# Performance work log

Measured on AMD Instinct MI355X. Metric: run time of the kernel, lower is better.

## Reference

```python
import jax, jax.numpy as jnp
import numpy as np

B, T, SEG = 64, 16, 50          # batch, n segments, segment length (cap 50 in original)
E, D, H, F = 512, 512, 8, 2048  # dim_embeddings, dim_encoder, n_heads, dim_ff
DH = D // H
SCALE = float(1.0 / np.sqrt(DH))


def _ln(x, g, b):
    m = jnp.mean(x, -1, keepdims=True)
    v = jnp.var(x, -1, keepdims=True)
    return (x - m) * jax.lax.rsqrt(v + 1e-5) * g + b


def _mha(q_in, kv_in, Wq, Wk, Wv, Wo, kv_lens):
    b, sq, _ = q_in.shape
    sk = kv_in.shape[1]
    q = (q_in @ Wq).reshape(b, sq, H, DH)
    k = (kv_in @ Wk).reshape(b, sk, H, DH)
    v = (kv_in @ Wv).reshape(b, sk, H, DH)
    scores = jnp.einsum('bqhd,bkhd->bhqk', q, k) * SCALE
    mask = jnp.arange(sk)[None, :] < kv_lens[:, None]  # [b, sk] key-padding mask
    scores = jnp.where(mask[:, None, None, :], scores, -1e9)
    a = jax.nn.softmax(scores, axis=-1)
    o = jnp.einsum('bhqk,bkhd->bqhd', a, v).reshape(b, sq, D)
    return o @ Wo


def _ffn(x, W1, W2):
    return jax.nn.relu(x @ W1) @ W2


def _encoder(x, lens, p):
    # TransformerEncoder: project E->D, masked self-attn + FFN, post-LN residuals
    h = x @ p['eWin']
    h = _ln(h + _mha(h, h, p['eWq'], p['eWk'], p['eWv'], p['eWo'], lens), p['eG1'], p['eB1'])
    return _ln(h + _ffn(h, p['eF1'], p['eF2']), p['eG2'], p['eB2'])


def _connection(prev, curr, prev_lens, p):
    # Connection: curr cross-attends over prev (masked by prev_lens) + FFN
    h = _ln(curr + _mha(curr, prev, p['cWq'], p['cWk'], p['cWv'], p['cWo'], prev_lens), p['cG1'], p['cB1'])
    return _ln(h + _ffn(h, p['cF1'], p['cF2']), p['cG2'], p['cB2'])


def _forward(seqs, ends, p):
    first_lens = jnp.minimum(ends[:, 0], SEG)
    encoded = _encoder(seqs[:, :SEG], first_lens, p)  # [B, SEG, D]
    # regular segmentation: ends[b,t] = (t+1)*SEG, so every step uses a full segment
    segs = seqs.reshape(B, T, SEG, E).transpose(1, 0, 2, 3)[1:]        # [T-1, B, SEG, E]
    seg_lens = jnp.minimum(ends[:, 1:] - ends[:, :-1], SEG).T          # [T-1, B]
    prev_lens = jnp.full((B,), SEG, jnp.int32)

    def step(enc, xs):
        seg, lens = xs
        currs = _encoder(seg, lens, p)
        out = _connection(enc, currs, prev_lens, p)
        return out, None  # out[-SEG:] == out since seq_len = min(diff, 50) = SEG

    encoded, _ = jax.lax.scan(step, encoded, (segs, seg_lens))
    return encoded


def setup_inputs():
    key = jax.random.key(0)
    ks = jax.random.split(key, 16)
    g = lambda k, s: jax.random.normal(k, s, jnp.float32) * 0.02
    inp = {
        'seqs': jax.random.normal(ks[0], (B, T * SEG, E), jnp.float32),
        'ends': jnp.broadcast_to((jnp.arange(1, T + 1) * SEG).astype(jnp.int32), (B, T)),
        'eWin': g(ks[1], (E, D)),
        'eWq': g(ks[2], (D, D)), 'eWk': g(ks[3], (D, D)),
        'eWv': g(ks[4], (D, D)), 'eWo': g(ks[5], (D, D)),
        'eG1': jnp.ones(D), 'eB1': jnp.zeros(D),
        'eF1': g(ks[6], (D, F)), 'eF2': g(ks[7], (F, D)),
        'eG2': jnp.ones(D), 'eB2': jnp.zeros(D),
        'cWq': g(ks[8], (D, D)), 'cWk': g(ks[9], (D, D)),
        'cWv': g(ks[10], (D, D)), 'cWo': g(ks[11], (D, D)),
        'cG1': jnp.ones(D), 'cB1': jnp.zeros(D),
        'cF1': g(ks[12], (D, F)), 'cF2': g(ks[13], (F, D)),
        'cG2': jnp.ones(D), 'cB2': jnp.zeros(D),
    }
    return inp


def reference(seqs, ends, eWin, eWq, eWk, eWv, eWo, eG1, eB1, eF1, eF2, eG2, eB2,
              cWq, cWk, cWv, cWo, cG1, cB1, cF1, cF2, cG2, cB2):
    p = dict(eWin=eWin, eWq=eWq, eWk=eWk, eWv=eWv, eWo=eWo, eG1=eG1, eB1=eB1,
             eF1=eF1, eF2=eF2, eG2=eG2, eB2=eB2, cWq=cWq, cWk=cWk, cWv=cWv,
             cWo=cWo, cG1=cG1, cB1=cB1, cF1=cF1, cF2=cF2, cG2=cG2, cB2=cB2)
    return _forward(seqs, ends, p)
```

## Files before the change

### kernel.cpp

```cpp
#include <hip/hip_runtime.h>


#define NB   64
#define NT   16
#define SEGL 50
#define DMODEL 512
#define DFF  2048
#define NHEAD 8
#define DHEAD 64

typedef unsigned short ushort_t;
typedef __attribute__((ext_vector_type(8))) short bfrag;
typedef __attribute__((ext_vector_type(4))) float ffrag;

__device__ __forceinline__ ushort_t f2b(float x) {
    union { float f; unsigned u; } c; c.f = x;
    unsigned r = c.u + 0x7fffu + ((c.u >> 16) & 1u);
    return (ushort_t)(r >> 16);
}

#define GLOAD_LDS16(g, l) __builtin_amdgcn_global_load_lds( \
    (const __attribute__((address_space(1))) void*)(g),      \
    (__attribute__((address_space(3))) void*)(l), 16, 0, 0)

template<int BM, int BN, int WROWS, int WCOLS>
__global__ __launch_bounds__(256) void mfma_gemm(
    const ushort_t* __restrict__ A, int agrp, long long astride,
    const ushort_t* __restrict__ Bt, ushort_t* __restrict__ C,
    int M, int N, int K, int relu)
{
    constexpr int WM = BM / WROWS, WN = BN / WCOLS;
    constexpr int SM = WM / 16, SN = WN / 16;
    constexpr int NSUBA = BM / 16, NSUBB = BN / 16;
    constexpr int NSUB = NSUBA + NSUBB;
    constexpr int SPW = NSUB / 4;
    __shared__ ushort_t lds[NSUB * 512];

    const int tid = threadIdx.x;
    const int wave = tid >> 6, lane = tid & 63;
    const int wrow = wave / WCOLS, wcol = wave % WCOLS;
    const int bm = blockIdx.y * BM, bn = blockIdx.x * BN;
    const int lm = lane & 15, lq = lane >> 4;

    ffrag acc[SM][SN];
#pragma unroll
    for (int i = 0; i < SM; ++i)
#pragma unroll
        for (int j = 0; j < SN; ++j) acc[i][j] = (ffrag){0.f, 0.f, 0.f, 0.f};

    const ushort_t* gptr[SPW];
    ushort_t* lptr[SPW];
#pragma unroll
    for (int i = 0; i < SPW; ++i) {
        int s = wave * SPW + i;
        if (s < NSUBA) {
            int m = bm + s * 16 + lm;
            gptr[i] = A + (long long)(m / agrp) * astride
                        + (long long)(m % agrp) * K + lq * 8;
        } else {
            int n = bn + (s - NSUBA) * 16 + lm;
            gptr[i] = Bt + (long long)n * K + lq * 8;
        }
        lptr[i] = &lds[s * 512];
    }

    for (int kk = 0; kk < K; kk += 32) {
        __syncthreads();
#pragma unroll
        for (int i = 0; i < SPW; ++i)
            GLOAD_LDS16(gptr[i] + kk, lptr[i]);
        __builtin_amdgcn_s_waitcnt(0);
        __syncthreads();

        bfrag af[SM], bfg[SN];
#pragma unroll
        for (int i = 0; i < SM; ++i)
            af[i] = *(const bfrag*)&lds[(wrow * SM + i) * 512 + lane * 8];
#pragma unroll
        for (int j = 0; j < SN; ++j)
            bfg[j] = *(const bfrag*)&lds[(NSUBA + wcol * SN + j) * 512 + lane * 8];
#pragma unroll
        for (int i = 0; i < SM; ++i)
#pragma unroll
            for (int j = 0; j < SN; ++j)
                acc[i][j] = __builtin_amdgcn_mfma_f32_16x16x32_bf16(
                    af[i], bfg[j], acc[i][j], 0, 0, 0);
    }

#pragma unroll
    for (int i = 0; i < SM; ++i)
#pragma unroll
        for (int j = 0; j < SN; ++j) {
            int col = bn + wcol * WN + j * 16 + lm;
#pragma unroll
            for (int r = 0; r < 4; ++r) {
                int row = bm + wrow * WM + i * 16 + lq * 4 + r;
                float v = acc[i][j][r];
                if (relu) v = fmaxf(v, 0.f);
                C[(long long)row * N + col] = f2b(v);
            }
        }
}

__global__ __launch_bounds__(256) void wtrans_k(
    const float* __restrict__ W, ushort_t* __restrict__ Wt, int K, int N)
{
    __shared__ float t[32][33];
    const int bk = blockIdx.y * 32, bn = blockIdx.x * 32;
    const int tx = threadIdx.x & 31, ty = threadIdx.x >> 5;
    for (int i = ty; i < 32; i += 8)
        t[i][tx] = W[(long long)(bk + i) * N + bn + tx];
    __syncthreads();
    for (int i = ty; i < 32; i += 8)
        Wt[(long long)(bn + i) * K + bk + tx] = f2b(t[tx][i]);
}

__global__ __launch_bounds__(256) void cvt_k(
    const float* __restrict__ in, ushort_t* __restrict__ out, long long n)
{
    long long i = ((long long)blockIdx.x * 256 + threadIdx.x) * 8;
    if (i >= n) return;
    float4 a = *(const float4*)(in + i);
    float4 b = *(const float4*)(in + i + 4);
    ushort_t o[8] = {f2b(a.x), f2b(a.y), f2b(a.z), f2b(a.w),
                     f2b(b.x), f2b(b.y), f2b(b.z), f2b(b.w)};
    *(uint4*)(out + i) = *(const uint4*)o;
}

__global__ __launch_bounds__(256) void attn_mfma_k(
    const ushort_t* __restrict__ Q, long long qns, long long qrs,
    const ushort_t* __restrict__ K, const ushort_t* __restrict__ V,
    long long kns, long long kvrs,
    ushort_t* __restrict__ O,
    const int* __restrict__ lens, int G, int t0)
{
    __shared__ ushort_t qs[64][72];
    __shared__ ushort_t ks[64][72];
    __shared__ ushort_t vt[64][72];
    const int n = blockIdx.x >> 3, h = blockIdx.x & 7;
    const int tid = threadIdx.x;
    const int wave = tid >> 6, lane = tid & 63;
    const int lm = lane & 15, lq = lane >> 4;
    int len = SEGL;
    if (lens) {
        int b = n / G, t = t0 + (n % G);
        len = lens[b * NT + t];
        if (len > SEGL) len = SEGL;
    }
    {
        uint4 z = {0, 0, 0, 0};
        uint4* vz = (uint4*)&vt[0][0];
        for (int i = tid; i < 64 * 72 / 8; i += 256) vz[i] = z;
    }
    __syncthreads();
    for (int idx = tid; idx < SEGL * 8; idx += 256) {
        int s = idx >> 3, d8 = (idx & 7) << 3;
        const ushort_t* qp = Q + (long long)n * qns + (long long)s * qrs + h * DHEAD + d8;
        const ushort_t* kp = K + (long long)n * kns + (long long)s * kvrs + h * DHEAD + d8;
        const ushort_t* vp = V + (long long)n * kns + (long long)s * kvrs + h * DHEAD + d8;
        *(uint4*)&qs[s][d8] = *(const uint4*)qp;
        *(uint4*)&ks[s][d8] = *(const uint4*)kp;
        uint4 v4 = *(const uint4*)vp;
        const ushort_t* vv = (const ushort_t*)&v4;
#pragma unroll
        for (int u = 0; u < 8; ++u) vt[d8 + u][s] = vv[u];
    }
    __syncthreads();

    ffrag sc[4];
#pragma unroll
    for (int nt = 0; nt < 4; ++nt) sc[nt] = (ffrag){0.f, 0.f, 0.f, 0.f};
#pragma unroll
    for (int kt = 0; kt < 2; ++kt) {
        bfrag a = *(const bfrag*)&qs[wave * 16 + lm][kt * 32 + lq * 8];
#pragma unroll
        for (int nt = 0; nt < 4; ++nt) {
            bfrag b = *(const bfrag*)&ks[nt * 16 + lm][kt * 32 + lq * 8];
            sc[nt] = __builtin_amdgcn_mfma_f32_16x16x32_bf16(a, b, sc[nt], 0, 0, 0);
        }
    }
    __syncthreads();

#pragma unroll
    for (int r = 0; r < 4; ++r) {
        float x[4];
        float mx = -1e30f;
#pragma unroll
        for (int nt = 0; nt < 4; ++nt) {
            int col = nt * 16 + lm;
            x[nt] = (col < len) ? sc[nt][r] * 0.125f : -1e9f;
            mx = fmaxf(mx, x[nt]);
        }
        for (int off = 8; off; off >>= 1) mx = fmaxf(mx, __shfl_xor(mx, off));
        float e[4], se = 0.f;
#pragma unroll
        for (int nt = 0; nt < 4; ++nt) { e[nt] = __expf(x[nt] - mx); se += e[nt]; }
        for (int off = 8; off; off >>= 1) se += __shfl_xor(se, off);
        float inv = 1.f / se;
        int row = wave * 16 + lq * 4 + r;
#pragma unroll
        for (int nt = 0; nt < 4; ++nt)
            qs[row][nt * 16 + lm] = f2b(e[nt] * inv);
    }
    __syncthreads();

    ffrag oc[4];
#pragma unroll
    for (int dt = 0; dt < 4; ++dt) oc[dt] = (ffrag){0.f, 0.f, 0.f, 0.f};
#pragma unroll
    for (int kt = 0; kt < 2; ++kt) {
        bfrag a = *(const bfrag*)&qs[wave * 16 + lm][kt * 32 + lq * 8];
#pragma unroll
        for (int dt = 0; dt < 4; ++dt) {
            bfrag b = *(const bfrag*)&vt[dt * 16 + lm][kt * 32 + lq * 8];
            oc[dt] = __builtin_amdgcn_mfma_f32_16x16x32_bf16(a, b, oc[dt], 0, 0, 0);
        }
    }
#pragma unroll
    for (int r = 0; r < 4; ++r) {
        int i = wave * 16 + lq * 4 + r;
        if (i < SEGL) {
            ushort_t* op = O + (long long)(n * SEGL + i) * DMODEL + h * DHEAD + lm;
#pragma unroll
            for (int dt = 0; dt < 4; ++dt)
                op[dt * 16] = f2b(oc[dt][r]);
        }
    }
}

template<bool OUTF32>
__global__ __launch_bounds__(256) void add_ln_k(
    const ushort_t* __restrict__ A, int agrp, long long astride,
    const ushort_t* __restrict__ Bv,
    const float* __restrict__ gamma, const float* __restrict__ beta,
    void* __restrict__ O, int ogrp, long long ostride, int M)
{
    const int wave = threadIdx.x >> 6, lane = threadIdx.x & 63;
    const int r = blockIdx.x * 4 + wave;
    if (r >= M) return;
    const ushort_t* a = A + (long long)(r / agrp) * astride + (long long)(r % agrp) * DMODEL;
    const ushort_t* b = Bv + (long long)r * DMODEL;
    float x[8];
    {
        uint4 a4 = *(const uint4*)(a + lane * 8);
        uint4 b4 = *(const uint4*)(b + lane * 8);
        const unsigned* aa = (const unsigned*)&a4;
        const unsigned* bb = (const unsigned*)&b4;
#pragma unroll
        for (int c = 0; c < 4; ++c) {
            union { unsigned u; float f; } alo, ahi, blo, bhi;
            alo.u = aa[c] << 16; ahi.u = aa[c] & 0xffff0000u;
            blo.u = bb[c] << 16; bhi.u = bb[c] & 0xffff0000u;
            x[2 * c]     = alo.f + blo.f;
            x[2 * c + 1] = ahi.f + bhi.f;
        }
    }
    float s = 0.f, s2 = 0.f;
#pragma unroll
    for (int i = 0; i < 8; ++i) { s += x[i]; s2 = fmaf(x[i], x[i], s2); }
    for (int off = 32; off; off >>= 1) {
        s += __shfl_xor(s, off);
        s2 += __shfl_xor(s2, off);
    }
    const float mean = s * (1.f / DMODEL);
    const float var = s2 * (1.f / DMODEL) - mean * mean;
    const float inv = rsqrtf(var + 1e-5f);
    float4 g0 = *(const float4*)(gamma + lane * 8);
    float4 g1 = *(const float4*)(gamma + lane * 8 + 4);
    float4 be0 = *(const float4*)(beta + lane * 8);
    float4 be1 = *(const float4*)(beta + lane * 8 + 4);
    float y[8];
    y[0] = (x[0] - mean) * inv * g0.x + be0.x;
    y[1] = (x[1] - mean) * inv * g0.y + be0.y;
    y[2] = (x[2] - mean) * inv * g0.z + be0.z;
    y[3] = (x[3] - mean) * inv * g0.w + be0.w;
    y[4] = (x[4] - mean) * inv * g1.x + be1.x;
    y[5] = (x[5] - mean) * inv * g1.y + be1.y;
    y[6] = (x[6] - mean) * inv * g1.z + be1.z;
    y[7] = (x[7] - mean) * inv * g1.w + be1.w;
    if (OUTF32) {
        float* o = (float*)O + (long long)(r / ogrp) * ostride + (long long)(r % ogrp) * DMODEL;
        *(float4*)(o + lane * 8) = *(float4*)&y[0];
        *(float4*)(o + lane * 8 + 4) = *(float4*)&y[4];
    } else {
        ushort_t* o = (ushort_t*)O + (long long)(r / ogrp) * ostride + (long long)(r % ogrp) * DMODEL;
        ushort_t ob[8];
#pragma unroll
        for (int i = 0; i < 8; ++i) ob[i] = f2b(y[i]);
        *(uint4*)(o + lane * 8) = *(const uint4*)ob;
    }
}

__global__ void lens_k(const int* __restrict__ ends, int* __restrict__ lens)
{
    int i = blockIdx.x * 256 + threadIdx.x;
    if (i >= NB * NT) return;
    int t = i & (NT - 1);
    int prev = t ? ends[i - 1] : 0;
    int l = ends[i] - prev;
    if (l > SEGL) l = SEGL;
    lens[i] = l;
}

extern "C" void kernel_launch(void* const* d_in, const int* in_sizes, int n_in,
                              void* d_out, int out_size, void* d_ws, size_t ws_size,
                              hipStream_t stream)
{
    const float* seqs = (const float*)d_in[0];
    const int*   ends = (const int*)d_in[1];
    const float* eG1 = (const float*)d_in[7],  *eB1 = (const float*)d_in[8];
    const float* eG2 = (const float*)d_in[11], *eB2 = (const float*)d_in[12];
    const float* cG1 = (const float*)d_in[17], *cB1 = (const float*)d_in[18];
    const float* cG2 = (const float*)d_in[21], *cB2 = (const float*)d_in[22];
    float* out = (float*)d_out;

    ushort_t* ws = (ushort_t*)d_ws;
    const long long SEQROW = (long long)NT * SEGL * DMODEL;
    ushort_t* SEQB = ws;
    ushort_t* WT   = SEQB + 26214400LL;
    ushort_t* ENC  = WT   + 6553600LL;
    ushort_t* BUF0 = ENC  + 26214400LL;
    ushort_t* QKV  = BUF0 + 6553600LL;
    ushort_t* BUF4 = QKV  + 19660800LL;
    ushort_t* BUF1 = BUF4 + 6553600LL;
    ushort_t* BUF2 = BUF1 + 6553600LL;
    ushort_t* MID  = BUF2 + 6553600LL;
    ushort_t* OUTB = MID  + 26214400LL;
    ushort_t* QALL = OUTB + 1638400LL;
    int*      lens = (int*)(QALL + 24576000LL);

    const ushort_t* eWinT = WT + 0;
    const ushort_t* WQKVe = WT + 262144;
    const ushort_t* eWoT  = WT + 1048576;
    const ushort_t* eF1T  = WT + 1310720;
    const ushort_t* eF2T  = WT + 2359296;
    const ushort_t* cWqT  = WT + 3407872;
    const ushort_t* cKV   = WT + 3670016;
    const ushort_t* cWoT  = WT + 4194304;
    const ushort_t* cF1T  = WT + 4456448;
    const ushort_t* cF2T  = WT + 5505024;

    struct WMap { int src; long long dst; int K, N; };
    const WMap wm[13] = {
        {2,  0,       512, 512},
        {3,  262144,  512, 512},
        {4,  524288,  512, 512},
        {5,  786432,  512, 512},
        {6,  1048576, 512, 512},
        {9,  1310720, 512, 2048},
        {10, 2359296, 2048, 512},
        {13, 3407872, 512, 512},
        {14, 3670016, 512, 512},
        {15, 3932160, 512, 512},
        {16, 4194304, 512, 512},
        {19, 4456448, 512, 2048},
        {20, 5505024, 2048, 512},
    };

    cvt_k<<<12800, 256, 0, stream>>>(seqs, SEQB, 26214400LL);
    for (int w = 0; w < 13; ++w) {
        dim3 g(wm[w].N / 32, wm[w].K / 32);
        wtrans_k<<<g, 256, 0, stream>>>((const float*)d_in[wm[w].src],
                                        WT + wm[w].dst, wm[w].K, wm[w].N);
    }
    lens_k<<<4, 256, 0, stream>>>(ends, lens);

    auto gemmL = [&](const ushort_t* A, int agrp, long long astr, const ushort_t* Bt,
                     ushort_t* C, int M, int N, int K, int relu) {
        dim3 g(N / 128, M / 128);
        mfma_gemm<128, 128, 2, 2><<<g, 256, 0, stream>>>(A, agrp, astr, Bt, C, M, N, K, relu);
    };
    auto gemmS = [&](const ushort_t* A, int agrp, long long astr, const ushort_t* Bt,
                     ushort_t* C, int M, int N, int K, int relu) {
        dim3 g(N / 128, M / 64);
        mfma_gemm<64, 128, 2, 2><<<g, 256, 0, stream>>>(A, agrp, astr, Bt, C, M, N, K, relu);
    };

    const int G = 4;
    const int Mc = NB * G * SEGL;
    for (int c = 0; c < NT / G; ++c) {
        const int t0 = c * G;
        const ushort_t* Abase = SEQB + (long long)t0 * SEGL * DMODEL;
        ushort_t* ENCc = ENC + (long long)t0 * SEGL * DMODEL;
        gemmL(Abase, G * SEGL, SEQROW, eWinT, BUF0, Mc, 512, 512, 0);
        gemmL(BUF0, Mc, 0, WQKVe, QKV, Mc, 1536, 512, 0);
        attn_mfma_k<<<NB * G * NHEAD, 256, 0, stream>>>(
            QKV, 50LL * 1536, 1536, QKV + 512, QKV + 1024, 50LL * 1536, 1536,
            BUF4, lens, G, t0);
        gemmL(BUF4, Mc, 0, eWoT, BUF1, Mc, 512, 512, 0);
        add_ln_k<false><<<Mc / 4, 256, 0, stream>>>(BUF0, Mc, 0, BUF1, eG1, eB1,
                                                    BUF2, Mc, 0, Mc);
        gemmL(BUF2, Mc, 0, eF1T, MID, Mc, 2048, 512, 1);
        gemmL(MID, Mc, 0, eF2T, BUF1, Mc, 512, 2048, 0);
        add_ln_k<false><<<Mc / 4, 256, 0, stream>>>(BUF2, Mc, 0, BUF1, eG2, eB2,
                                                    ENCc, G * SEGL, SEQROW, Mc);
    }

    gemmL(ENC + 25600, 750, SEQROW, cWqT, QALL, 48000, 512, 512, 0);

    const int Ms = NB * SEGL;
    for (int t = 1; t < NT; ++t) {
        const ushort_t* currA = ENC + (long long)t * SEGL * DMODEL;
        const ushort_t* prevA; int pg; long long ps;
        if (t == 1) { prevA = ENC;  pg = SEGL; ps = SEQROW; }
        else        { prevA = OUTB; pg = Ms;   ps = 0; }
        gemmS(prevA, pg, ps, cKV, QKV, Ms, 1024, 512, 0);
        attn_mfma_k<<<NB * NHEAD, 256, 0, stream>>>(
            QALL + (long long)(t - 1) * 25600, 750LL * 512, 512,
            QKV, QKV + 512, 50LL * 1024, 1024,
            BUF4, nullptr, 1, 0);
        gemmS(BUF4, Ms, 0, cWoT, BUF0, Ms, 512, 512, 0);
        add_ln_k<false><<<Ms / 4, 256, 0, stream>>>(currA, SEGL, SEQROW, BUF0, cG1, cB1,
                                                    BUF2, Ms, 0, Ms);
        gemmS(BUF2, Ms, 0, cF1T, MID, Ms, 2048, 512, 1);
        gemmS(MID, Ms, 0, cF2T, BUF0, Ms, 512, 2048, 0);
        if (t == NT - 1)
            add_ln_k<true><<<Ms / 4, 256, 0, stream>>>(BUF2, Ms, 0, BUF0, cG2, cB2,
                                                       out, Ms, 0, Ms);
        else
            add_ln_k<false><<<Ms / 4, 256, 0, stream>>>(BUF2, Ms, 0, BUF0, cG2, cB2,
                                                        OUTB, Ms, 0, Ms);
    }
}
```

Baseline: 3.154 ms.

## Double-buffer GEMM LDS tiles and vectorize epilogue stores via LDS staging

The MFMA GEMM now uses two LDS buffers, so global-to-LDS loads for the next K slice are issued before the MFMAs on the current slice. This drops the explicit wait plus second barrier per iteration and overlaps memory latency with compute. The epilogue writes the bf16 results into a padded per-wave LDS tile, then copies them to global memory as 16-byte coalesced stores instead of scattered 2-byte stores. The cost is double the LDS footprint, which may lower occupancy. Correctness relies on the barrier waiting for the outstanding LDS-direct loads.

```diff
diff --git a/kernel.cpp b/kernel.cpp
--- a/kernel.cpp
+++ b/kernel.cpp
@@ -34,7 +34,11 @@
     constexpr int NSUBA = BM / 16, NSUBB = BN / 16;
     constexpr int NSUB = NSUBA + NSUBB;
     constexpr int SPW = NSUB / 4;
-    __shared__ ushort_t lds[NSUB * 512];
+    constexpr int EST = WN + 8;
+    constexpr int LDS_KLOOP = 2 * NSUB * 512;
+    constexpr int LDS_EPI   = 4 * WM * EST;
+    constexpr int LDS_SZ = LDS_KLOOP > LDS_EPI ? LDS_KLOOP : LDS_EPI;
+    __shared__ ushort_t lds[LDS_SZ];
 
     const int tid = threadIdx.x;
     const int wave = tid >> 6, lane = tid & 63;
@@ -49,7 +53,6 @@
         for (int j = 0; j < SN; ++j) acc[i][j] = (ffrag){0.f, 0.f, 0.f, 0.f};
 
     const ushort_t* gptr[SPW];
-    ushort_t* lptr[SPW];
 #pragma unroll
     for (int i = 0; i < SPW; ++i) {
         int s = wave * SPW + i;
@@ -61,24 +64,31 @@
             int n = bn + (s - NSUBA) * 16 + lm;
             gptr[i] = Bt + (long long)n * K + lq * 8;
         }
-        lptr[i] = &lds[s * 512];
-    }
-
-    for (int kk = 0; kk < K; kk += 32) {
+    }
+
+#pragma unroll
+    for (int i = 0; i < SPW; ++i)
+        GLOAD_LDS16(gptr[i], &lds[(wave * SPW + i) * 512]);
+
+    const int nk = K >> 5;
+    for (int kk = 0; kk < nk; ++kk) {
         __syncthreads();
-#pragma unroll
-        for (int i = 0; i < SPW; ++i)
-            GLOAD_LDS16(gptr[i] + kk, lptr[i]);
-        __builtin_amdgcn_s_waitcnt(0);
-        __syncthreads();
-
+        if (kk + 1 < nk) {
+            const int koff = (kk + 1) << 5;
+            const int nb = (kk + 1) & 1;
+#pragma unroll
+            for (int i = 0; i < SPW; ++i)
+                GLOAD_LDS16(gptr[i] + koff,
+                            &lds[nb * (NSUB * 512) + (wave * SPW + i) * 512]);
+        }
+        const ushort_t* lb = &lds[(kk & 1) * (NSUB * 512)];
         bfrag af[SM], bfg[SN];
 #pragma unroll
         for (int i = 0; i < SM; ++i)
-            af[i] = *(const bfrag*)&lds[(wrow * SM + i) * 512 + lane * 8];
+            af[i] = *(const bfrag*)&lb[(wrow * SM + i) * 512 + lane * 8];
 #pragma unroll
         for (int j = 0; j < SN; ++j)
-            bfg[j] = *(const bfrag*)&lds[(NSUBA + wcol * SN + j) * 512 + lane * 8];
+            bfg[j] = *(const bfrag*)&lb[(NSUBA + wcol * SN + j) * 512 + lane * 8];
 #pragma unroll
         for (int i = 0; i < SM; ++i)
 #pragma unroll
@@ -87,19 +97,31 @@
                     af[i], bfg[j], acc[i][j], 0, 0, 0);
     }
 
+    __syncthreads();
+    ushort_t* ep = &lds[wave * WM * EST];
 #pragma unroll
     for (int i = 0; i < SM; ++i)
 #pragma unroll
-        for (int j = 0; j < SN; ++j) {
-            int col = bn + wcol * WN + j * 16 + lm;
+        for (int j = 0; j < SN; ++j)
 #pragma unroll
             for (int r = 0; r < 4; ++r) {
-                int row = bm + wrow * WM + i * 16 + lq * 4 + r;
+                int row = i * 16 + lq * 4 + r;
+                int col = j * 16 + lm;
                 float v = acc[i][j][r];
                 if (relu) v = fmaxf(v, 0.f);
-                C[(long long)row * N + col] = f2b(v);
+                ep[row * EST + col] = f2b(v);
             }
-        }
+    constexpr int CPR = WN / 8;
+    constexpr int RPI = 64 / CPR;
+    const int lrow = lane / CPR, lcol = (lane % CPR) * 8;
+#pragma unroll
+    for (int it = 0; it < WM / RPI; ++it) {
+        int row = it * RPI + lrow;
+        uint4 v = *(const uint4*)&ep[row * EST + lcol];
+        long long grow = bm + wrow * WM + row;
+        int gcol = bn + wcol * WN + lcol;
+        *(uint4*)&C[grow * N + gcol] = v;
+    }
 }
 
 __global__ __launch_bounds__(256) void wtrans_k(
```

Result: faster. 2.851 ms (-9.6%).
